# Kernel optimization log

Measured on AMD Instinct MI355X. Metric: run time of the kernel, lower is better.

## Reference

```python
import jax, jax.numpy as jnp
import numpy as np

TYPE_NUM = 4
CHILDS = [2, 2, 2, 2]
NODE_NUM = 8          # sum(CHILDS)
HEADS = 4
GROUP = 4
IN, MID, OUT = 256, 256, 256


def _mask():
    m = np.zeros((TYPE_NUM, NODE_NUM), np.float32)
    s = 0
    for i, c in enumerate(CHILDS):
        m[i, s:s + c] = 1.0
        s += c
    return jnp.asarray(m)


def _graph_feature(x, node_num):
    # x: [B, L, C] -> [B, M, node_num+1, C] with M = (L-1)//node_num
    B, L, C = x.shape
    node_x = x[:, 1:, :].reshape(B, -1, C * node_num)
    M = node_x.shape[1]
    src = x[:, :M, :]
    return jnp.concatenate([node_x, src], axis=2).reshape(B, M, node_num + 1, C)


def _conv1d(x, w, b, groups):
    # x: [N, C, T], w: [O, C//groups, K], stride == K, 'VALID' -> length-1 output
    y = jax.lax.conv_general_dilated(
        x, w, window_strides=(w.shape[-1],), padding='VALID',
        feature_group_count=groups, dimension_numbers=('NCH', 'OIH', 'NCH'))
    return y + b[None, :, None]


def _agg(feat, attn, mask):
    # feat: [B, M, node_num+1, C]; attn: [B, M, node_num, HEADS] (softmaxed)
    B, M, A, C = feat.shape
    n = A - 1
    nf = feat[:, :, :-1, :].reshape(B, M, n, HEADS, C // HEADS) * attn[..., None]
    nf = nf.reshape(B, M, n, C)
    agg = jnp.einsum('tn,bmnc->bmtc', mask, nf)  # masked group-sum (bmm with block mask)
    return agg, feat[:, :, -1, :]


def setup_inputs() -> dict:
    key = jax.random.key(0)
    ks = jax.random.split(key, 12)
    B, L = 4, 32777

    def lin(k, fi, fo):
        return jax.random.normal(k, (fi, fo), jnp.float32) / np.sqrt(fi).astype(np.float32)

    def convw(k, o, i, kk):
        return jax.random.normal(k, (o, i, kk), jnp.float32) / np.sqrt(i * kk).astype(np.float32)

    return {
        'input': jax.random.normal(ks[0], (B, L, IN), jnp.float32),
        'gt': jax.random.normal(ks[1], (B, 512, IN), jnp.float32),
        'w_att': lin(ks[2], IN, HEADS), 'b_att': jnp.zeros((HEADS,), jnp.float32),
        'w_gt1': lin(ks[3], IN, MID), 'b_gt1': jnp.zeros((MID,), jnp.float32),
        'w_gt2': lin(ks[4], MID, OUT), 'b_gt2': jnp.zeros((OUT,), jnp.float32),
        'w_agg1': convw(ks[5], MID, IN // GROUP, TYPE_NUM), 'b_agg1': jnp.zeros((MID,), jnp.float32),
        'w_src1': convw(ks[6], MID, IN // GROUP, 1), 'b_src1': jnp.zeros((MID,), jnp.float32),
        'w_agg2': convw(ks[7], OUT, MID // GROUP, TYPE_NUM), 'b_agg2': jnp.zeros((OUT,), jnp.float32),
        'w_src2': convw(ks[8], OUT, MID // GROUP, 1), 'b_src2': jnp.zeros((OUT,), jnp.float32),
    }


def reference(input, gt, w_att, b_att, w_gt1, b_gt1, w_gt2, b_gt2,
              w_agg1, b_agg1, w_src1, b_src1, w_agg2, b_agg2, w_src2, b_src2):
    mask = _mask()
    B = gt.shape[0]
    # gt branch (eval mode: dropout = identity)
    gt1 = jax.nn.relu(gt @ w_gt1 + b_gt1)   # [B, 512, MID]
    gt2 = jax.nn.relu(gt1 @ w_gt2 + b_gt2)  # [B, 512, OUT]

    # ---- layer 1 ----
    feat = _graph_feature(input, NODE_NUM)   # [B, M, 9, IN]
    M = feat.shape[1]
    ft = feat[:, :, -1:, :] + feat[:, :, :-1, :]          # source + each neighbor
    attn = jax.nn.softmax(ft @ w_att + b_att, axis=2)     # softmax over node dim
    node, src = _agg(feat, attn, mask)                    # [B,M,T,IN], [B,M,IN]
    BM = B * M
    node = jnp.transpose(node.reshape(BM, TYPE_NUM, IN), (0, 2, 1))  # [BM, IN, T]
    src = src.reshape(BM, IN, 1)
    node1 = jax.nn.relu(_conv1d(node, w_agg1, b_agg1, GROUP))[:, :, 0]  # [BM, MID]
    src1 = jax.nn.relu(_conv1d(src, w_src1, b_src1, GROUP))[:, :, 0]

    nf1 = node1.reshape(B, M, MID)[:, 0, :]
    d1 = gt1[:, 0, :] - nf1
    score1 = 1.0 - jnp.exp(-0.5 * jnp.sum(d1 * d1, axis=1))  # [B]

    out1 = (node1 + src1).reshape(B, M, MID)

    # ---- layer 2 (reuses attn truncated to M2) ----
    feat2 = _graph_feature(out1, NODE_NUM)  # [B, M2, 9, MID]
    M2 = feat2.shape[1]
    node2, src2 = _agg(feat2, attn[:, :M2], mask)
    BM2 = B * M2
    node2 = jnp.transpose(node2.reshape(BM2, TYPE_NUM, MID), (0, 2, 1))
    src2 = src2.reshape(BM2, MID, 1)
    node2c = jax.nn.relu(_conv1d(node2, w_agg2, b_agg2, GROUP))  # [BM2, OUT, 1]

    nf2 = node2c.reshape(B, M2, OUT)
    d2 = (gt2[:, :M2, :] - nf2).reshape(-1, OUT)
    score2 = 1.0 - jnp.exp(-0.5 * jnp.sum(d2 * d2, axis=1))  # [B*M2]

    src2c = jax.nn.relu(_conv1d(src2, w_src2, b_src2, GROUP))
    output = (node2c + src2c).reshape(-1, OUT)  # [B*M2, OUT]
    return output, score1, score2
```

## Files before the change

### kernel.cpp

```cpp
#include <hip/hip_runtime.h>
#include <hip/hip_bf16.h>

typedef unsigned short u16;
typedef unsigned int   u32;
typedef __attribute__((ext_vector_type(8))) short short8;
typedef __attribute__((ext_vector_type(4))) float f32x4;

#define BB  4
#define LL  32777
#define MM  4097
#define MMP 4112
#define MM2 512

__device__ __forceinline__ float b2f(u16 u) { return __uint_as_float(((u32)u) << 16); }
__device__ __forceinline__ u16 f2bf(float f) {
    u32 u = __float_as_uint(f);
    return (u16)((u + 0x7fffu + ((u >> 16) & 1u)) >> 16);
}
__device__ __forceinline__ u32 pk(float a, float b) {
    union { __hip_bfloat162 h; u32 u; } cv;
    cv.h = __float22bfloat162_rn(make_float2(a, b));
    return cv.u;
}
__device__ __forceinline__ float bflo(u32 u) { return __uint_as_float(u << 16); }
__device__ __forceinline__ float bfhi(u32 u) { return __uint_as_float(u & 0xffff0000u); }

__global__ __launch_bounds__(256) void setup_k(
    const float* __restrict__ wagg1, const float* __restrict__ wagg2,
    const float* __restrict__ wsrc1, const float* __restrict__ wsrc2,
    const float* __restrict__ watt,
    u16* __restrict__ wA1, u16* __restrict__ wA2,
    u16* __restrict__ wS1, u16* __restrict__ wS2, u16* __restrict__ wattB) {
    int idx = blockIdx.x * 256 + threadIdx.x;
    if (idx < 131072) {
        int which = idx >> 16;
        int e = idx & 65535;
        int j = e & 7, lane = (e >> 3) & 63, mt = (e >> 9) & 3, kc = (e >> 11) & 7, g = (e >> 14) & 3;
        int ol = mt * 16 + (lane & 15);
        int k = kc * 32 + (lane >> 4) * 8 + j;
        int t = k >> 6, ci = k & 63;
        const float* src = which ? wagg2 : wagg1;
        u16* dst = which ? wA2 : wA1;
        dst[e] = f2bf(src[(g * 64 + ol) * 256 + ci * 4 + t]);
    } else if (idx < 163840) {
        int e2 = idx - 131072;
        int which = e2 >> 14;
        int e = e2 & 16383;
        int j = e & 7, lane = (e >> 3) & 63, mt = (e >> 9) & 3, kc = (e >> 11) & 1, g = (e >> 12) & 3;
        int ol = mt * 16 + (lane & 15);
        int k = kc * 32 + (lane >> 4) * 8 + j;
        const float* src = which ? wsrc2 : wsrc1;
        u16* dst = which ? wS2 : wS1;
        dst[e] = f2bf(src[(g * 64 + ol) * 64 + k]);
    } else {
        int e = idx - 163840;
        int j = e & 7, lane = (e >> 3) & 63, kc = e >> 9;
        int h = lane & 15, quad = lane >> 4;
        int k = kc * 32 + quad * 8 + j;
        wattB[e] = (h < 4) ? f2bf(watt[k * 4 + h]) : (u16)0;
    }
}

__global__ __launch_bounds__(256, 4) void l1fused_k(
    const float* __restrict__ x, const float* __restrict__ batt,
    const u16* __restrict__ wA1, const u16* __restrict__ wS1,
    const u16* __restrict__ wattB,
    const float* __restrict__ bagg1, const float* __restrict__ bsrc1,
    float* __restrict__ attnf, u16* __restrict__ out1, float* __restrict__ n1m0,
    const float* __restrict__ gt, const float* __restrict__ W1, const float* __restrict__ b1,
    const float* __restrict__ W2, const float* __restrict__ b2,
    float* __restrict__ gt2, float* __restrict__ gt1m0) {
    __shared__ u16   sh_node[64 * 256];
    __shared__ u16   sh_srcq[8 * 256];
    __shared__ float shR[576];

    int tid = threadIdx.x;
    int b = blockIdx.y;

    if (blockIdx.x >= 513) {
        float (*sh)[8] = (float(*)[8])sh_node;
        int gi = (blockIdx.x - 513) * 4 + b;
        int row0 = gi * 8;
        {
            int r = tid >> 5, j = tid & 31;
            const float4* a4 = (const float4*)(gt + (size_t)(row0 + r) * 256 + j * 8);
            float4 v0 = a4[0], v1 = a4[1];
            sh[j * 8 + 0][r] = v0.x; sh[j * 8 + 1][r] = v0.y;
            sh[j * 8 + 2][r] = v0.z; sh[j * 8 + 3][r] = v0.w;
            sh[j * 8 + 4][r] = v1.x; sh[j * 8 + 5][r] = v1.y;
            sh[j * 8 + 6][r] = v1.z; sh[j * 8 + 7][r] = v1.w;
        }
        __syncthreads();
        int o = tid;
        float acc[8];
        {
            float bo = b1[o];
            #pragma unroll
            for (int i = 0; i < 8; ++i) acc[i] = bo;
        }
        #pragma unroll 4
        for (int k = 0; k < 256; ++k) {
            float wv = W1[k * 256 + o];
            const float4* ap = (const float4*)&sh[k][0];
            float4 a0 = ap[0], a1 = ap[1];
            acc[0] = fmaf(a0.x, wv, acc[0]); acc[1] = fmaf(a0.y, wv, acc[1]);
            acc[2] = fmaf(a0.z, wv, acc[2]); acc[3] = fmaf(a0.w, wv, acc[3]);
            acc[4] = fmaf(a1.x, wv, acc[4]); acc[5] = fmaf(a1.y, wv, acc[5]);
            acc[6] = fmaf(a1.z, wv, acc[6]); acc[7] = fmaf(a1.w, wv, acc[7]);
        }
        #pragma unroll
        for (int i = 0; i < 8; ++i) acc[i] = fmaxf(acc[i], 0.f);
        if ((row0 & 511) == 0) gt1m0[(row0 >> 9) * 256 + o] = acc[0];
        __syncthreads();
        #pragma unroll
        for (int i = 0; i < 8; ++i) sh[o][i] = acc[i];
        __syncthreads();
        {
            float bo = b2[o];
            #pragma unroll
            for (int i = 0; i < 8; ++i) acc[i] = bo;
        }
        #pragma unroll 4
        for (int k = 0; k < 256; ++k) {
            float wv = W2[k * 256 + o];
            const float4* ap = (const float4*)&sh[k][0];
            float4 a0 = ap[0], a1 = ap[1];
            acc[0] = fmaf(a0.x, wv, acc[0]); acc[1] = fmaf(a0.y, wv, acc[1]);
            acc[2] = fmaf(a0.z, wv, acc[2]); acc[3] = fmaf(a0.w, wv, acc[3]);
            acc[4] = fmaf(a1.x, wv, acc[4]); acc[5] = fmaf(a1.y, wv, acc[5]);
            acc[6] = fmaf(a1.z, wv, acc[6]); acc[7] = fmaf(a1.w, wv, acc[7]);
        }
        #pragma unroll
        for (int i = 0; i < 8; ++i) gt2[(size_t)(row0 + i) * 256 + o] = fmaxf(acc[i], 0.f);
        return;
    }

    int lane = tid & 63, w = tid >> 6;
    int quad = lane >> 4;
    int p0 = blockIdx.x * 8;

    {
        int rslot = tid >> 4, cseg = tid & 15;
        const float* xb = x + (size_t)b * LL * 256;
        #pragma unroll
        for (int pass = 0; pass < 5; ++pass) {
            int r = pass * 16 + rslot;
            if (r < 72) {
                int grow, key; u16* dst;
                if (r < 64) {
                    int pos = r >> 3, nn = r & 7;
                    int gp = p0 + pos; int gpc = gp < MM ? gp : MM - 1;
                    grow = 1 + 8 * gpc + nn;
                    dst = sh_node + r * 256;
                    key = (pos ^ nn) & 7;
                } else {
                    int q = r - 64;
                    int gp = p0 + q; int gpc = gp < MM ? gp : MM - 1;
                    grow = gpc;
                    dst = sh_srcq + q * 256;
                    key = q & 7;
                }
                const float4* src4 = (const float4*)(xb + (size_t)grow * 256 + cseg * 16);
                float4 v0 = src4[0], v1 = src4[1], v2 = src4[2], v3 = src4[3];
                uint4 o0, o1;
                o0.x = pk(v0.x, v0.y); o0.y = pk(v0.z, v0.w);
                o0.z = pk(v1.x, v1.y); o0.w = pk(v1.z, v1.w);
                o1.x = pk(v2.x, v2.y); o1.y = pk(v2.z, v2.w);
                o1.z = pk(v3.x, v3.y); o1.w = pk(v3.z, v3.w);
                int cb0 = cseg * 2;
                *(uint4*)(dst + ((cb0 ^ key) * 8))       = o0;
                *(uint4*)(dst + (((cb0 + 1) ^ key) * 8)) = o1;
            }
        }
    }
    __syncthreads();

    {
        short8 wB[8];
        #pragma unroll
        for (int kc = 0; kc < 8; ++kc) wB[kc] = *(const short8*)(wattB + kc * 512 + lane * 8);
        int m = lane & 15;
        int h = lane & 15;
        {
            int r = w * 16 + m;
            int key = ((r >> 3) ^ (r & 7)) & 7;
            const u16* rowp = sh_node + r * 256;
            f32x4 acc = (f32x4){0.f, 0.f, 0.f, 0.f};
            #pragma unroll
            for (int kc = 0; kc < 8; ++kc) {
                int cb = kc * 4 + quad;
                short8 aF = *(const short8*)(rowp + ((cb ^ key) * 8));
                acc = __builtin_amdgcn_mfma_f32_16x16x32_bf16(aF, wB[kc], acc, 0, 0, 0);
            }
            if (h < 4) {
                #pragma unroll
                for (int r2 = 0; r2 < 4; ++r2)
                    shR[(w * 16 + quad * 4 + r2) * 4 + h] = acc[r2];
            }
        }
        if (w == 3) {
            int ms = m < 8 ? m : 7;
            int key = ms & 7;
            const u16* rowp = sh_srcq + ms * 256;
            f32x4 acc = (f32x4){0.f, 0.f, 0.f, 0.f};
            #pragma unroll
            for (int kc = 0; kc < 8; ++kc) {
                int cb = kc * 4 + quad;
                short8 aF = *(const short8*)(rowp + ((cb ^ key) * 8));
                acc = __builtin_amdgcn_mfma_f32_16x16x32_bf16(aF, wB[kc], acc, 0, 0, 0);
            }
            if (h < 4) {
                #pragma unroll
                for (int r2 = 0; r2 < 4; ++r2) {
                    int rr = quad * 4 + r2;
                    if (rr < 8) shR[256 + rr * 4 + h] = acc[r2];
                }
            }
        }
    }
    __syncthreads();

    if (tid < 32) {
        int q = tid >> 2, h = tid & 3;
        float base = shR[256 + q * 4 + h] + batt[h];
        float l[8], mx = -3.0e38f;
        #pragma unroll
        for (int n = 0; n < 8; ++n) { l[n] = shR[(q * 8 + n) * 4 + h] + base; mx = fmaxf(mx, l[n]); }
        float s = 0.f;
        #pragma unroll
        for (int n = 0; n < 8; ++n) { l[n] = __expf(l[n] - mx); s += l[n]; }
        float inv = 1.f / s;
        int gp = p0 + q;
        float* at = shR + 320;
        #pragma unroll
        for (int n = 0; n < 8; ++n) {
            float aa = l[n] * inv;
            at[(n * 4 + h) * 8 + q] = aa;
            if (gp < MM2) attnf[(((size_t)b * MM2 + gp) * 8 + n) * 4 + h] = aa;
        }
    }
    __syncthreads();

    int g = w;
    int col = lane & 15;
    int pos = col & 7;
    float aT[8];
    {
        const float* at = shR + 320;
        #pragma unroll
        for (int nn = 0; nn < 8; ++nn) aT[nn] = at[(nn * 4 + g) * 8 + pos];
    }
    f32x4 accn[4], accs[4];
    #pragma unroll
    for (int mt = 0; mt < 4; ++mt) { accn[mt] = (f32x4){0,0,0,0}; accs[mt] = (f32x4){0,0,0,0}; }

    #pragma unroll
    for (int kc = 0; kc < 8; ++kc) {
        int k0 = kc * 32 + quad * 8;
        int t = k0 >> 6, ci0 = k0 & 63;
        int cb = (g * 64 + ci0) >> 3;
        int r0 = pos * 8 + 2 * t;
        int key0 = (pos ^ (2 * t)) & 7, key1 = (pos ^ (2 * t + 1)) & 7;
        short8 n0 = *(const short8*)(sh_node + r0 * 256 + ((cb ^ key0) * 8));
        short8 n1 = *(const short8*)(sh_node + (r0 + 1) * 256 + ((cb ^ key1) * 8));
        float a0 = aT[2 * t], a1 = aT[2 * t + 1];
        union { uint4 u; short8 s; } cv;
        #pragma unroll
        for (int e = 0; e < 4; ++e) {
            float lo = fmaf(a0, b2f((u16)n0[2 * e]),     a1 * b2f((u16)n1[2 * e]));
            float hi = fmaf(a0, b2f((u16)n0[2 * e + 1]), a1 * b2f((u16)n1[2 * e + 1]));
            ((u32*)&cv.u)[e] = pk(lo, hi);
        }
        short8 bB = cv.s;
        #pragma unroll
        for (int mt = 0; mt < 4; ++mt) {
            short8 aA = *(const short8*)(wA1 + (((g * 8 + kc) * 4 + mt) * 512 + lane * 8));
            accn[mt] = __builtin_amdgcn_mfma_f32_16x16x32_bf16(aA, bB, accn[mt], 0, 0, 0);
        }
    }
    #pragma unroll
    for (int kc = 0; kc < 2; ++kc) {
        int cb = (g * 64 + kc * 32 + quad * 8) >> 3;
        short8 bS = *(const short8*)(sh_srcq + pos * 256 + ((cb ^ pos) * 8));
        #pragma unroll
        for (int mt = 0; mt < 4; ++mt) {
            short8 aS = *(const short8*)(wS1 + (((g * 2 + kc) * 4 + mt) * 512 + lane * 8));
            accs[mt] = __builtin_amdgcn_mfma_f32_16x16x32_bf16(aS, bS, accs[mt], 0, 0, 0);
        }
    }
    __syncthreads();

    u16* outt = sh_srcq;
    #pragma unroll
    for (int mt = 0; mt < 4; ++mt) {
        int ob = g * 64 + mt * 16 + quad * 4;
        float v[4], n1v[4];
        #pragma unroll
        for (int r = 0; r < 4; ++r) {
            int o = ob + r;
            float n1 = fmaxf(accn[mt][r] + bagg1[o], 0.f);
            float s1 = fmaxf(accs[mt][r] + bsrc1[o], 0.f);
            n1v[r] = n1;
            v[r] = n1 + s1;
        }
        if (col < 8) {
            u32* wp = (u32*)&outt[col * 256 + ob];
            wp[0] = pk(v[0], v[1]);
            wp[1] = pk(v[2], v[3]);
        }
        if (blockIdx.x == 0 && col == 0) {
            #pragma unroll
            for (int r = 0; r < 4; ++r) n1m0[b * 256 + ob + r] = n1v[r];
        }
    }
    __syncthreads();
    {
        int posw = tid >> 5, cc = (tid & 31) * 8;
        if (p0 + posw < MM)
            *(uint4*)&out1[((size_t)b * MMP + p0 + posw) * 256 + cc] = *(const uint4*)&outt[posw * 256 + cc];
    }
}

__global__ __launch_bounds__(256) void l2conv_k(
    const u16* __restrict__ out1, const float* __restrict__ attnf,
    const float* __restrict__ gt2,
    const u16* __restrict__ wA2, const u16* __restrict__ wS2,
    const float* __restrict__ bagg2, const float* __restrict__ bsrc2,
    const float* __restrict__ gt1m0, const float* __restrict__ n1m0,
    float* __restrict__ outp, float* __restrict__ score2p, float* __restrict__ score1p) {
    __shared__ char shraw[16 * 268 * 4 * 2];
    __shared__ float shred[128];

    int tid = threadIdx.x;
    int b = blockIdx.y;

    if (blockIdx.x == 64) {
        float d = gt1m0[b * 256 + tid] - n1m0[b * 256 + tid];
        float v = d * d;
        #pragma unroll
        for (int off = 32; off > 0; off >>= 1) v += __shfl_down(v, off, 64);
        if ((tid & 63) == 0) shred[tid >> 6] = v;
        __syncthreads();
        if (tid == 0) score1p[b] = 1.f - __expf(-0.5f * (shred[0] + shred[1] + shred[2] + shred[3]));
        return;
    }

    int p0 = blockIdx.x * 8;
    u16* aggl = (u16*)shraw;

    {
        int pos16 = tid >> 4, cc = tid & 15;
        int pos = pos16 < 8 ? pos16 : 7;
        int m = p0 + pos;
        int c0 = cc * 16;
        int h = c0 >> 6;
        const float* arow = attnf + ((size_t)b * MM2 + m) * 32;
        #pragma unroll
        for (int t = 0; t < 4; ++t) {
            float a0 = arow[(2 * t) * 4 + h];
            float a1 = arow[(2 * t + 1) * 4 + h];
            const uint4* r0 = (const uint4*)(out1 + ((size_t)b * MMP + 1 + 8 * m + 2 * t) * 256 + c0);
            const uint4* r1 = (const uint4*)(out1 + ((size_t)b * MMP + 2 + 8 * m + 2 * t) * 256 + c0);
            u32 w[8];
            #pragma unroll
            for (int v = 0; v < 2; ++v) {
                uint4 p = r0[v], q = r1[v];
                u32 pv[4] = {p.x, p.y, p.z, p.w};
                u32 qv[4] = {q.x, q.y, q.z, q.w};
                #pragma unroll
                for (int e = 0; e < 4; ++e) {
                    float lo = fmaf(bflo(pv[e]), a0, bflo(qv[e]) * a1);
                    float hi = fmaf(bfhi(pv[e]), a0, bfhi(qv[e]) * a1);
                    w[v * 4 + e] = pk(lo, hi);
                }
            }
            u32* dst = (u32*)&aggl[pos16 * 1024 + h * 256 + t * 64 + (c0 & 63)];
            ((uint4*)dst)[0] = make_uint4(w[0], w[1], w[2], w[3]);
            ((uint4*)dst)[1] = make_uint4(w[4], w[5], w[6], w[7]);
        }
    }
    __syncthreads();

    int lane = tid & 63, g = tid >> 6;
    int col = lane & 15, quad = lane >> 4;
    f32x4 accn[4], accs[4];
    #pragma unroll
    for (int mt = 0; mt < 4; ++mt) { accn[mt] = (f32x4){0,0,0,0}; accs[mt] = (f32x4){0,0,0,0}; }

    #pragma unroll
    for (int kc = 0; kc < 8; ++kc) {
        short8 bB = *(const short8*)&aggl[col * 1024 + g * 256 + kc * 32 + quad * 8];
        #pragma unroll
        for (int mt = 0; mt < 4; ++mt) {
            short8 aA = *(const short8*)(wA2 + (((g * 8 + kc) * 4 + mt) * 512 + lane * 8));
            accn[mt] = __builtin_amdgcn_mfma_f32_16x16x32_bf16(aA, bB, accn[mt], 0, 0, 0);
        }
    }
    {
        int pcol = col < 8 ? col : 7;
        #pragma unroll
        for (int kc = 0; kc < 2; ++kc) {
            short8 bS = *(const short8*)(out1 + ((size_t)b * MMP + p0 + pcol) * 256 + g * 64 + kc * 32 + quad * 8);
            #pragma unroll
            for (int mt = 0; mt < 4; ++mt) {
                short8 aS = *(const short8*)(wS2 + (((g * 2 + kc) * 4 + mt) * 512 + lane * 8));
                accs[mt] = __builtin_amdgcn_mfma_f32_16x16x32_bf16(aS, bS, accs[mt], 0, 0, 0);
            }
        }
    }
    __syncthreads();

    float* outt = (float*)shraw;
    float* n2t  = outt + 16 * 268;
    #pragma unroll
    for (int mt = 0; mt < 4; ++mt) {
        #pragma unroll
        for (int r = 0; r < 4; ++r) {
            int o = g * 64 + mt * 16 + quad * 4 + r;
            float n2 = fmaxf(accn[mt][r] + bagg2[o], 0.f);
            float s2 = fmaxf(accs[mt][r] + bsrc2[o], 0.f);
            outt[col * 268 + o] = n2 + s2;
            n2t[col * 268 + o] = n2;
        }
    }
    __syncthreads();

    for (int j = tid; j < 512; j += 256) {
        int pos = j >> 6, cc = (j & 63) * 4;
        *(float4*)&outp[((size_t)b * MM2 + p0 + pos) * 256 + cc] = *(const float4*)&outt[pos * 268 + cc];
    }
    if (tid < 128) {
        int pos = tid >> 4, kk = tid & 15;
        const float* grow = gt2 + ((size_t)b * MM2 + p0 + pos) * 256 + kk * 16;
        const float* nrow = n2t + pos * 268 + kk * 16;
        float s = 0.f;
        #pragma unroll
        for (int c = 0; c < 16; ++c) { float d = grow[c] - nrow[c]; s = fmaf(d, d, s); }
        shred[pos * 16 + kk] = s;
    }
    __syncthreads();
    if (tid < 8) {
        float s = 0.f;
        #pragma unroll
        for (int kk = 0; kk < 16; ++kk) s += shred[tid * 16 + kk];
        score2p[(size_t)b * MM2 + p0 + tid] = 1.f - __expf(-0.5f * s);
    }
}

extern "C" void kernel_launch(void* const* d_in, const int* in_sizes, int n_in,
                              void* d_out, int out_size, void* d_ws, size_t ws_size,
                              hipStream_t stream) {
    const float* x     = (const float*)d_in[0];
    const float* gt    = (const float*)d_in[1];
    const float* watt  = (const float*)d_in[2];
    const float* batt  = (const float*)d_in[3];
    const float* wgt1  = (const float*)d_in[4];
    const float* bgt1  = (const float*)d_in[5];
    const float* wgt2  = (const float*)d_in[6];
    const float* bgt2  = (const float*)d_in[7];
    const float* wagg1 = (const float*)d_in[8];
    const float* bagg1 = (const float*)d_in[9];
    const float* wsrc1 = (const float*)d_in[10];
    const float* bsrc1 = (const float*)d_in[11];
    const float* wagg2 = (const float*)d_in[12];
    const float* bagg2 = (const float*)d_in[13];
    const float* wsrc2 = (const float*)d_in[14];
    const float* bsrc2 = (const float*)d_in[15];

    char* ws = (char*)d_ws;
    float* ws_gt2  = (float*)(ws + 0);
    float* attnf   = (float*)(ws + 2097152);
    float* n1m0    = (float*)(ws + 2359296);
    float* gt1m0   = (float*)(ws + 2363392);
    u16*   wA1     = (u16*)(ws + 2367488);
    u16*   wS1     = (u16*)(ws + 2498560);
    u16*   wA2     = (u16*)(ws + 2531328);
    u16*   wS2     = (u16*)(ws + 2662400);
    u16*   wattB   = (u16*)(ws + 2695168);
    u16*   out1    = (u16*)(ws + 2703360);

    float* outp    = (float*)d_out;
    float* score1p = outp + 524288;
    float* score2p = outp + 524292;

    setup_k<<<dim3(656), dim3(256), 0, stream>>>(wagg1, wagg2, wsrc1, wsrc2, watt,
                                                 wA1, wA2, wS1, wS2, wattB);
    l1fused_k<<<dim3(577, 4), dim3(256), 0, stream>>>(x, batt, wA1, wS1, wattB, bagg1, bsrc1,
                                                      attnf, out1, n1m0,
                                                      gt, wgt1, bgt1, wgt2, bgt2, ws_gt2, gt1m0);
    l2conv_k<<<dim3(65, 4), dim3(256), 0, stream>>>(out1, attnf, ws_gt2, wA2, wS2, bagg2, bsrc2,
                                                    gt1m0, n1m0, outp, score2p, score1p);
}
```

Measured before the change: 277.9 us.

## Reorder gt blocks first, batch global loads, prefetch weights, halve layer-2 tile

Moves the gt MLP blocks to the front of the layer-1 grid so the slow tail blocks start early. It also issues all x loads before the bf16 packing and loads the attention weights before the barrier. Conv weight fragments are double-buffered across k-chunks in both kernels, and the layer-2 kernel now handles 4 positions per block instead of 8, doubling its grid for more parallelism. The cost is higher register pressure and redundant padded work in the smaller layer-2 tiles.

```diff
diff --git a/kernel.cpp b/kernel.cpp
--- a/kernel.cpp
+++ b/kernel.cpp
@@ -77,9 +77,9 @@
     int tid = threadIdx.x;
     int b = blockIdx.y;
 
-    if (blockIdx.x >= 513) {
+    if (blockIdx.x < 64) {
         float (*sh)[8] = (float(*)[8])sh_node;
-        int gi = (blockIdx.x - 513) * 4 + b;
+        int gi = blockIdx.x * 4 + b;
         int row0 = gi * 8;
         {
             int r = tid >> 5, j = tid & 31;
@@ -98,7 +98,7 @@
             #pragma unroll
             for (int i = 0; i < 8; ++i) acc[i] = bo;
         }
-        #pragma unroll 4
+        #pragma unroll 8
         for (int k = 0; k < 256; ++k) {
             float wv = W1[k * 256 + o];
             const float4* ap = (const float4*)&sh[k][0];
@@ -120,7 +120,7 @@
             #pragma unroll
             for (int i = 0; i < 8; ++i) acc[i] = bo;
         }
-        #pragma unroll 4
+        #pragma unroll 8
         for (int k = 0; k < 256; ++k) {
             float wv = W2[k * 256 + o];
             const float4* ap = (const float4*)&sh[k][0];
@@ -135,50 +135,66 @@
         return;
     }
 
+    int bx = blockIdx.x - 64;
     int lane = tid & 63, w = tid >> 6;
     int quad = lane >> 4;
-    int p0 = blockIdx.x * 8;
+    int p0 = bx * 8;
 
     {
         int rslot = tid >> 4, cseg = tid & 15;
         const float* xb = x + (size_t)b * LL * 256;
+        const float* srcA[5];
+        u16* dstA[5];
+        int keyA[5];
         #pragma unroll
         for (int pass = 0; pass < 5; ++pass) {
             int r = pass * 16 + rslot;
-            if (r < 72) {
-                int grow, key; u16* dst;
-                if (r < 64) {
-                    int pos = r >> 3, nn = r & 7;
-                    int gp = p0 + pos; int gpc = gp < MM ? gp : MM - 1;
-                    grow = 1 + 8 * gpc + nn;
-                    dst = sh_node + r * 256;
-                    key = (pos ^ nn) & 7;
-                } else {
-                    int q = r - 64;
-                    int gp = p0 + q; int gpc = gp < MM ? gp : MM - 1;
-                    grow = gpc;
-                    dst = sh_srcq + q * 256;
-                    key = q & 7;
-                }
-                const float4* src4 = (const float4*)(xb + (size_t)grow * 256 + cseg * 16);
-                float4 v0 = src4[0], v1 = src4[1], v2 = src4[2], v3 = src4[3];
+            int grow, key; u16* dst;
+            if (r < 64) {
+                int pos = r >> 3, nn = r & 7;
+                int gp = p0 + pos; int gpc = gp < MM ? gp : MM - 1;
+                grow = 1 + 8 * gpc + nn;
+                dst = sh_node + r * 256;
+                key = (pos ^ nn) & 7;
+            } else {
+                int q = r - 64;
+                int qq = q < 8 ? q : 7;
+                int gp = p0 + qq; int gpc = gp < MM ? gp : MM - 1;
+                grow = gpc;
+                dst = sh_srcq + qq * 256;
+                key = qq & 7;
+            }
+            srcA[pass] = xb + (size_t)grow * 256 + cseg * 16;
+            dstA[pass] = dst;
+            keyA[pass] = key;
+        }
+        float4 v0[5], v1[5], v2[5], v3[5];
+        #pragma unroll
+        for (int pass = 0; pass < 5; ++pass) {
+            const float4* s4 = (const float4*)srcA[pass];
+            v0[pass] = s4[0]; v1[pass] = s4[1]; v2[pass] = s4[2]; v3[pass] = s4[3];
+        }
+        #pragma unroll
+        for (int pass = 0; pass < 5; ++pass) {
+            bool val = (pass < 4) || (rslot < 8);
+            if (val) {
                 uint4 o0, o1;
-                o0.x = pk(v0.x, v0.y); o0.y = pk(v0.z, v0.w);
-                o0.z = pk(v1.x, v1.y); o0.w = pk(v1.z, v1.w);
-                o1.x = pk(v2.x, v2.y); o1.y = pk(v2.z, v2.w);
-                o1.z = pk(v3.x, v3.y); o1.w = pk(v3.z, v3.w);
-                int cb0 = cseg * 2;
-                *(uint4*)(dst + ((cb0 ^ key) * 8))       = o0;
-                *(uint4*)(dst + (((cb0 + 1) ^ key) * 8)) = o1;
-            }
-        }
-    }
-    __syncthreads();
-
-    {
-        short8 wB[8];
-        #pragma unroll
-        for (int kc = 0; kc < 8; ++kc) wB[kc] = *(const short8*)(wattB + kc * 512 + lane * 8);
+                o0.x = pk(v0[pass].x, v0[pass].y); o0.y = pk(v0[pass].z, v0[pass].w);
+                o0.z = pk(v1[pass].x, v1[pass].y); o0.w = pk(v1[pass].z, v1[pass].w);
+                o1.x = pk(v2[pass].x, v2[pass].y); o1.y = pk(v2[pass].z, v2[pass].w);
+                o1.z = pk(v3[pass].x, v3[pass].y); o1.w = pk(v3[pass].z, v3[pass].w);
+                int cb0 = cseg * 2, key = keyA[pass];
+                *(uint4*)(dstA[pass] + ((cb0 ^ key) * 8))       = o0;
+                *(uint4*)(dstA[pass] + (((cb0 + 1) ^ key) * 8)) = o1;
+            }
+        }
+    }
+    short8 wB[8];
+    #pragma unroll
+    for (int kc = 0; kc < 8; ++kc) wB[kc] = *(const short8*)(wattB + kc * 512 + lane * 8);
+    __syncthreads();
+
+    {
         int m = lane & 15;
         int h = lane & 15;
         {
@@ -254,8 +270,18 @@
     #pragma unroll
     for (int mt = 0; mt < 4; ++mt) { accn[mt] = (f32x4){0,0,0,0}; accs[mt] = (f32x4){0,0,0,0}; }
 
+    const u16* wAb = wA1 + (size_t)(g * 8) * 4 * 512 + lane * 8;
+    short8 aAc[4];
+    #pragma unroll
+    for (int mt = 0; mt < 4; ++mt) aAc[mt] = *(const short8*)(wAb + mt * 512);
+
     #pragma unroll
     for (int kc = 0; kc < 8; ++kc) {
+        short8 aAn[4];
+        if (kc < 7) {
+            #pragma unroll
+            for (int mt = 0; mt < 4; ++mt) aAn[mt] = *(const short8*)(wAb + ((kc + 1) * 4 + mt) * 512);
+        }
         int k0 = kc * 32 + quad * 8;
         int t = k0 >> 6, ci0 = k0 & 63;
         int cb = (g * 64 + ci0) >> 3;
@@ -273,9 +299,11 @@
         }
         short8 bB = cv.s;
         #pragma unroll
-        for (int mt = 0; mt < 4; ++mt) {
-            short8 aA = *(const short8*)(wA1 + (((g * 8 + kc) * 4 + mt) * 512 + lane * 8));
-            accn[mt] = __builtin_amdgcn_mfma_f32_16x16x32_bf16(aA, bB, accn[mt], 0, 0, 0);
+        for (int mt = 0; mt < 4; ++mt)
+            accn[mt] = __builtin_amdgcn_mfma_f32_16x16x32_bf16(aAc[mt], bB, accn[mt], 0, 0, 0);
+        if (kc < 7) {
+            #pragma unroll
+            for (int mt = 0; mt < 4; ++mt) aAc[mt] = aAn[mt];
         }
     }
     #pragma unroll
@@ -308,7 +336,7 @@
             wp[0] = pk(v[0], v[1]);
             wp[1] = pk(v[2], v[3]);
         }
-        if (blockIdx.x == 0 && col == 0) {
+        if (bx == 0 && col == 0) {
             #pragma unroll
             for (int r = 0; r < 4; ++r) n1m0[b * 256 + ob + r] = n1v[r];
         }
@@ -334,7 +362,7 @@
     int tid = threadIdx.x;
     int b = blockIdx.y;
 
-    if (blockIdx.x == 64) {
+    if (blockIdx.x == 128) {
         float d = gt1m0[b * 256 + tid] - n1m0[b * 256 + tid];
         float v = d * d;
         #pragma unroll
@@ -345,33 +373,49 @@
         return;
     }
 
-    int p0 = blockIdx.x * 8;
+    int p0 = blockIdx.x * 4;
     u16* aggl = (u16*)shraw;
 
     {
         int pos16 = tid >> 4, cc = tid & 15;
-        int pos = pos16 < 8 ? pos16 : 7;
+        int pos = pos16 & 3;
         int m = p0 + pos;
         int c0 = cc * 16;
         int h = c0 >> 6;
         const float* arow = attnf + ((size_t)b * MM2 + m) * 32;
+        uint4 P0[4], P1[4], Q0[4], Q1[4];
+        float a0v[4], a1v[4];
         #pragma unroll
         for (int t = 0; t < 4; ++t) {
-            float a0 = arow[(2 * t) * 4 + h];
-            float a1 = arow[(2 * t + 1) * 4 + h];
             const uint4* r0 = (const uint4*)(out1 + ((size_t)b * MMP + 1 + 8 * m + 2 * t) * 256 + c0);
             const uint4* r1 = (const uint4*)(out1 + ((size_t)b * MMP + 2 + 8 * m + 2 * t) * 256 + c0);
+            P0[t] = r0[0]; P1[t] = r0[1];
+            Q0[t] = r1[0]; Q1[t] = r1[1];
+            a0v[t] = arow[(2 * t) * 4 + h];
+            a1v[t] = arow[(2 * t + 1) * 4 + h];
+        }
+        #pragma unroll
+        for (int t = 0; t < 4; ++t) {
+            float a0 = a0v[t], a1 = a1v[t];
             u32 w[8];
-            #pragma unroll
-            for (int v = 0; v < 2; ++v) {
-                uint4 p = r0[v], q = r1[v];
-                u32 pv[4] = {p.x, p.y, p.z, p.w};
-                u32 qv[4] = {q.x, q.y, q.z, q.w};
+            {
+                u32 pv[4] = {P0[t].x, P0[t].y, P0[t].z, P0[t].w};
+                u32 qv[4] = {Q0[t].x, Q0[t].y, Q0[t].z, Q0[t].w};
                 #pragma unroll
                 for (int e = 0; e < 4; ++e) {
                     float lo = fmaf(bflo(pv[e]), a0, bflo(qv[e]) * a1);
                     float hi = fmaf(bfhi(pv[e]), a0, bfhi(qv[e]) * a1);
-                    w[v * 4 + e] = pk(lo, hi);
+                    w[e] = pk(lo, hi);
+                }
+            }
+            {
+                u32 pv[4] = {P1[t].x, P1[t].y, P1[t].z, P1[t].w};
+                u32 qv[4] = {Q1[t].x, Q1[t].y, Q1[t].z, Q1[t].w};
+                #pragma unroll
+                for (int e = 0; e < 4; ++e) {
+                    float lo = fmaf(bflo(pv[e]), a0, bflo(qv[e]) * a1);
+                    float hi = fmaf(bfhi(pv[e]), a0, bfhi(qv[e]) * a1);
+                    w[4 + e] = pk(lo, hi);
                 }
             }
             u32* dst = (u32*)&aggl[pos16 * 1024 + h * 256 + t * 64 + (c0 & 63)];
@@ -387,17 +431,29 @@
     #pragma unroll
     for (int mt = 0; mt < 4; ++mt) { accn[mt] = (f32x4){0,0,0,0}; accs[mt] = (f32x4){0,0,0,0}; }
 
+    const u16* wAb = wA2 + (size_t)(g * 8) * 4 * 512 + lane * 8;
+    short8 aAc[4];
+    #pragma unroll
+    for (int mt = 0; mt < 4; ++mt) aAc[mt] = *(const short8*)(wAb + mt * 512);
+
     #pragma unroll
     for (int kc = 0; kc < 8; ++kc) {
+        short8 aAn[4];
+        if (kc < 7) {
+            #pragma unroll
+            for (int mt = 0; mt < 4; ++mt) aAn[mt] = *(const short8*)(wAb + ((kc + 1) * 4 + mt) * 512);
+        }
         short8 bB = *(const short8*)&aggl[col * 1024 + g * 256 + kc * 32 + quad * 8];
         #pragma unroll
-        for (int mt = 0; mt < 4; ++mt) {
-            short8 aA = *(const short8*)(wA2 + (((g * 8 + kc) * 4 + mt) * 512 + lane * 8));
-            accn[mt] = __builtin_amdgcn_mfma_f32_16x16x32_bf16(aA, bB, accn[mt], 0, 0, 0);
-        }
-    }
-    {
-        int pcol = col < 8 ? col : 7;
+        for (int mt = 0; mt < 4; ++mt)
+            accn[mt] = __builtin_amdgcn_mfma_f32_16x16x32_bf16(aAc[mt], bB, accn[mt], 0, 0, 0);
+        if (kc < 7) {
+            #pragma unroll
+            for (int mt = 0; mt < 4; ++mt) aAc[mt] = aAn[mt];
+        }
+    }
+    {
+        int pcol = col & 3;
         #pragma unroll
         for (int kc = 0; kc < 2; ++kc) {
             short8 bS = *(const short8*)(out1 + ((size_t)b * MMP + p0 + pcol) * 256 + g * 64 + kc * 32 + quad * 8);
@@ -425,11 +481,11 @@
     }
     __syncthreads();
 
-    for (int j = tid; j < 512; j += 256) {
-        int pos = j >> 6, cc = (j & 63) * 4;
+    {
+        int pos = tid >> 6, cc = (tid & 63) * 4;
         *(float4*)&outp[((size_t)b * MM2 + p0 + pos) * 256 + cc] = *(const float4*)&outt[pos * 268 + cc];
     }
-    if (tid < 128) {
+    if (tid < 64) {
         int pos = tid >> 4, kk = tid & 15;
         const float* grow = gt2 + ((size_t)b * MM2 + p0 + pos) * 256 + kk * 16;
         const float* nrow = n2t + pos * 268 + kk * 16;
@@ -439,7 +495,7 @@
         shred[pos * 16 + kk] = s;
     }
     __syncthreads();
-    if (tid < 8) {
+    if (tid < 4) {
         float s = 0.f;
         #pragma unroll
         for (int kk = 0; kk < 16; ++kk) s += shred[tid * 16 + kk];
@@ -488,6 +544,6 @@
     l1fused_k<<<dim3(577, 4), dim3(256), 0, stream>>>(x, batt, wA1, wS1, wattB, bagg1, bsrc1,
                                                       attnf, out1, n1m0,
                                                       gt, wgt1, bgt1, wgt2, bgt2, ws_gt2, gt1m0);
-    l2conv_k<<<dim3(65, 4), dim3(256), 0, stream>>>(out1, attnf, ws_gt2, wA2, wS2, bagg2, bsrc2,
-                                                    gt1m0, n1m0, outp, score2p, score1p);
+    l2conv_k<<<dim3(129, 4), dim3(256), 0, stream>>>(out1, attnf, ws_gt2, wA2, wS2, bagg2, bsrc2,
+                                                     gt1m0, n1m0, outp, score2p, score1p);
 }
```

Measured after the change: 251.4 us. -9.5%, faster.
